# Optimization experiments

Measured on AMD Instinct MI355X. Metric: run time of the kernel, lower is better.

## Reference

```python
import jax, jax.numpy as jnp
import numpy as np

B, N, T, F_IN = 16, 1024, 12, 1
D_MODEL, D_K, D_V, H, K = 512, 32, 32, 3, 3
C = 32  # nb_chev_filter == nb_time_filter


def _ln(x, g, b, eps=1e-5):
    mu = jnp.mean(x, -1, keepdims=True)
    var = jnp.var(x, -1, keepdims=True)
    return (x - mu) * jax.lax.rsqrt(var + eps) * g + b


def _conv(x, w, b):
    y = jax.lax.conv_general_dilated(x, w, (1, 1), 'VALID',
                                     dimension_numbers=('NCHW', 'OIHW', 'NCHW'))
    return y + b[None, :, None, None]


def setup_inputs() -> dict:
    key = jax.random.key(0)
    ks = iter(jax.random.split(key, 40))
    rn = lambda s, sc=0.02: jax.random.normal(next(ks), s, jnp.float32) * sc
    return dict(
        x=rn((B, N, F_IN, T), 1.0),
        res_att=rn((B, F_IN, H, T, T), 0.1),
        pos_embed_T=rn((T, N)),
        gamma_T=jnp.ones((N,)), beta_T=jnp.zeros((N,)),
        WQ_t=rn((N, D_K * H)), WK_t=rn((N, D_K * H)), WV_t=rn((N, D_V * H)),
        fc_t=rn((H * D_V, N)),
        pre_conv_w=rn((D_MODEL, T, 1, F_IN)), pre_conv_b=rn((D_MODEL,)),
        pos_embed_S=rn((N, D_MODEL)),
        gamma_S=jnp.ones((D_MODEL,)), beta_S=jnp.zeros((D_MODEL,)),
        WQ_s=rn((D_MODEL, D_K * K)), WK_s=rn((D_MODEL, D_K * K)),
        cheb_polys=rn((K, N, N), 0.05),
        adj_pa=(jax.random.uniform(next(ks), (N, N)) < 0.01).astype(jnp.float32),
        cheb_mask=rn((K, N, N)),
        Theta=rn((K, F_IN, C), 0.1),
        gtu3_w=rn((2 * C, C, 1, 3)), gtu3_b=rn((2 * C,)),
        gtu5_w=rn((2 * C, C, 1, 5)), gtu5_b=rn((2 * C,)),
        gtu7_w=rn((2 * C, C, 1, 7)), gtu7_b=rn((2 * C,)),
        res_conv_w=rn((C, F_IN, 1, 1)), res_conv_b=rn((C,)),
        fcmy_w=rn((3 * T - 12, T)), fcmy_b=rn((T,)),
        gamma_f=jnp.ones((C,)), beta_f=jnp.zeros((C,)),
    )


def reference(x, res_att, pos_embed_T, gamma_T, beta_T, WQ_t, WK_t, WV_t, fc_t,
              pre_conv_w, pre_conv_b, pos_embed_S, gamma_S, beta_S, WQ_s, WK_s,
              cheb_polys, adj_pa, cheb_mask, Theta,
              gtu3_w, gtu3_b, gtu5_w, gtu5_b, gtu7_w, gtu7_b,
              res_conv_w, res_conv_b, fcmy_w, fcmy_b, gamma_f, beta_f):
    B_, N_, F_, T_ = x.shape
    # ---- temporal embedding (num_of_features == 1 branch): (B,F,T,N) ----
    TEmx = _ln(jnp.transpose(x, (0, 2, 3, 1)) + pos_embed_T[None, None], gamma_T, beta_T)

    # ---- temporal MHA with residual attention bias ----
    def heads(e, W, d):
        y = e @ W  # (B,F,T,H*d)
        return jnp.transpose(y.reshape(B_, F_, T_, H, d), (0, 1, 3, 2, 4))  # (B,F,H,T,d)
    Q, Kt, V = heads(TEmx, WQ_t, D_K), heads(TEmx, WK_t, D_K), heads(TEmx, WV_t, D_V)
    re_At = jnp.einsum('bfhqd,bfhkd->bfhqk', Q, Kt) / np.sqrt(D_K) + res_att
    attn = jax.nn.softmax(re_At, axis=-1)
    ctx = jnp.einsum('bfhqk,bfhkd->bfhqd', attn, V)
    ctx = jnp.transpose(ctx, (0, 1, 3, 2, 4)).reshape(B_, F_, T_, H * D_V)
    one_n, zero_n = jnp.ones((N_,), x.dtype), jnp.zeros((N_,), x.dtype)
    TATout = _ln(ctx @ fc_t + TEmx, one_n, zero_n)  # fresh LayerNorm(d_model) -> gamma=1, beta=0

    # ---- pre_conv: Conv2d(T, d_model, kernel=(1,F)) on (B,T,N,F); take last col ----
    x_TAt = jnp.einsum('btnf,dtf->bnd', jnp.transpose(TATout, (0, 2, 3, 1)),
                       pre_conv_w[:, :, 0, :]) + pre_conv_b  # (B,N,d_model)

    # ---- spatial embedding + spatial attention scores (no softmax) ----
    SEmx = _ln(x_TAt + pos_embed_S[None], gamma_S, beta_S)  # dropout = identity (eval)
    Qs = jnp.transpose((SEmx @ WQ_s).reshape(B_, N_, K, D_K), (0, 2, 1, 3))
    Ks = jnp.transpose((SEmx @ WK_s).reshape(B_, N_, K, D_K), (0, 2, 1, 3))
    STAt = jnp.einsum('bknd,bkmd->bknm', Qs, Ks) / np.sqrt(D_K)  # (B,K,N,N)

    # ---- Chebyshev graph conv weighted by spatial attention ----
    satt = jax.nn.softmax(STAt + (adj_pa[None] * cheb_mask)[None], axis=2)
    Tka = cheb_polys[None] * satt  # (B,K,N,N)
    rhs = jnp.einsum('bkmn,bmft->bknft', Tka, x)  # T_k_with_at^T @ x over all t
    spatial_gcn = jax.nn.relu(jnp.einsum('bknft,kfo->bnot', rhs, Theta))  # (B,N,C,T)

    # ---- gated temporal convs (GTU) ----
    X = jnp.transpose(spatial_gcn, (0, 2, 1, 3))  # (B,C,N,T)
    def gtu(w, b):
        y = _conv(X, w, b)
        return jnp.tanh(y[:, :C]) * jax.nn.sigmoid(y[:, C:])
    time_conv = jnp.concatenate([gtu(gtu3_w, gtu3_b), gtu(gtu5_w, gtu5_b),
                                 gtu(gtu7_w, gtu7_b)], axis=-1)  # (B,C,N,3T-12)
    time_conv = time_conv @ fcmy_w + fcmy_b  # (B,C,N,T)
    tco = jax.nn.relu(time_conv)  # num_of_features == 1 branch

    # ---- residual 1x1 conv + final LayerNorm over channel dim ----
    x_res = _conv(jnp.transpose(x, (0, 2, 1, 3)), res_conv_w, res_conv_b)  # (B,C,N,T)
    out = _ln(jnp.transpose(jax.nn.relu(x_res + tco), (0, 3, 2, 1)), gamma_f, beta_f)
    out = jnp.transpose(out, (0, 2, 3, 1))  # (B,N,C,T)
    return out, re_At
```

## Files before the change

### kernel.cpp

```cpp
#include <hip/hip_runtime.h>
#include <hip/hip_bf16.h>
#include <math.h>

#define B_ 16
#define N_ 1024
#define T_ 12
#define DM_ 512
#define H_ 3
#define K_ 3
#define C_ 32
#define RSQRT_DK 0.17677669529663687f

typedef __attribute__((ext_vector_type(8))) short bf16x8;
typedef __attribute__((ext_vector_type(4))) float f32x4;

__device__ __forceinline__ ushort f2bf(float f) {
  uint u = __float_as_uint(f);
  return (ushort)((u + 0x7FFF + ((u >> 16) & 1)) >> 16);
}
__device__ __forceinline__ float bf2f(ushort h) {
  return __uint_as_float(((uint)h) << 16);
}

__global__ void k1_temporal_ln(const float* __restrict__ x, const float* __restrict__ posT,
                               const float* __restrict__ gT, const float* __restrict__ bT,
                               float* __restrict__ TEmx) {
  int row = blockIdx.x;
  int b = row / T_, t = row - b * T_;
  __shared__ float red[256], red2[256];
  float v[4]; float s = 0.f, s2 = 0.f;
  for (int i = 0; i < 4; ++i) {
    int n = threadIdx.x + (i << 8);
    float val = x[(b * N_ + n) * T_ + t] + posT[t * N_ + n];
    v[i] = val; s += val; s2 += val * val;
  }
  red[threadIdx.x] = s; red2[threadIdx.x] = s2;
  __syncthreads();
  for (int off = 128; off > 0; off >>= 1) {
    if (threadIdx.x < off) { red[threadIdx.x] += red[threadIdx.x + off]; red2[threadIdx.x] += red2[threadIdx.x + off]; }
    __syncthreads();
  }
  float mu = red[0] * (1.f / N_);
  float rs = rsqrtf(red2[0] * (1.f / N_) - mu * mu + 1e-5f);
  for (int i = 0; i < 4; ++i) {
    int n = threadIdx.x + (i << 8);
    TEmx[row * N_ + n] = (v[i] - mu) * rs * gT[n] + bT[n];
  }
}

__global__ __launch_bounds__(256) void k2_qkv(const float* __restrict__ TEmx,
                       const float* __restrict__ WQ, const float* __restrict__ WK,
                       const float* __restrict__ WV, float* __restrict__ part) {
  int kc = blockIdx.x, row = blockIdx.y;
  __shared__ float e[256];
  int tid = threadIdx.x;
  e[tid] = TEmx[row * N_ + kc * 256 + tid];
  __syncthreads();
  for (int col = tid; col < 288; col += 256) {
    int which = col / 96, j = col - which * 96;
    const float* W = (which == 0) ? WQ : ((which == 1) ? WK : WV);
    const float* Wp = W + (size_t)(kc * 256) * 96 + j;
    float acc = 0.f;
    #pragma unroll 8
    for (int n = 0; n < 256; ++n) acc += e[n] * Wp[n * 96];
    part[(row * 4 + kc) * 288 + col] = acc;
  }
}

__global__ __launch_bounds__(256) void k3a_attn(const float* __restrict__ part, const float* __restrict__ res_att,
                         float* __restrict__ reAt_out, float* __restrict__ ctx) {
  int bh = blockIdx.x;
  int b = bh / 3, h = bh - b * 3;
  __shared__ float q_l[3 * T_ * 32];
  __shared__ float s_l[T_ * T_];
  int tid = threadIdx.x;
  for (int i = tid; i < 1152; i += 256) {
    int sec = i / 384, r = i - sec * 384, t = r >> 5, d = r & 31;
    int col = sec * 96 + h * 32 + d;
    const float* pr = &part[(size_t)((b * T_ + t) * 4) * 288 + col];
    q_l[i] = pr[0] + pr[288] + pr[576] + pr[864];
  }
  __syncthreads();
  if (tid < 144) {
    int qi = tid / 12, ki = tid - qi * 12;
    float acc = 0.f;
    #pragma unroll
    for (int d = 0; d < 32; ++d)
      acc += q_l[qi * 32 + d] * q_l[384 + ki * 32 + d];
    float sv = acc * RSQRT_DK + res_att[(size_t)bh * 144 + tid];
    s_l[tid] = sv;
    reAt_out[(size_t)bh * 144 + tid] = sv;
  }
  __syncthreads();
  if (tid < 12) {
    float mx = -1e30f;
    for (int ki = 0; ki < 12; ++ki) mx = fmaxf(mx, s_l[tid * 12 + ki]);
    float sum = 0.f;
    for (int ki = 0; ki < 12; ++ki) { float p = __expf(s_l[tid * 12 + ki] - mx); s_l[tid * 12 + ki] = p; sum += p; }
    float inv = 1.f / sum;
    for (int ki = 0; ki < 12; ++ki) s_l[tid * 12 + ki] *= inv;
  }
  __syncthreads();
  for (int i = tid; i < 384; i += 256) {
    int qi = i >> 5, d = i & 31;
    float acc = 0.f;
    for (int ki = 0; ki < 12; ++ki)
      acc += s_l[qi * 12 + ki] * q_l[768 + ki * 32 + d];
    ctx[(size_t)(b * T_ + qi) * 96 + h * 32 + d] = acc;
  }
}

__global__ __launch_bounds__(1024) void k3b_tat(const float* __restrict__ ctx,
                        const float* __restrict__ fc_t,
                        const float* __restrict__ TEmx, float* __restrict__ TAT) {
  int row = blockIdx.x;
  __shared__ float c_l[96];
  __shared__ float red[16], red2[16];
  int tid = threadIdx.x;
  if (tid < 96) c_l[tid] = ctx[row * 96 + tid];
  __syncthreads();
  float acc = TEmx[row * N_ + tid];
  #pragma unroll 12
  for (int j = 0; j < 96; ++j) acc = fmaf(c_l[j], fc_t[j * N_ + tid], acc);
  float s = acc, s2 = acc * acc;
  #pragma unroll
  for (int off = 32; off > 0; off >>= 1) {
    s  += __shfl_xor(s, off);
    s2 += __shfl_xor(s2, off);
  }
  int w = tid >> 6;
  if ((tid & 63) == 0) { red[w] = s; red2[w] = s2; }
  __syncthreads();
  float ts = 0.f, ts2 = 0.f;
  #pragma unroll
  for (int i = 0; i < 16; ++i) { ts += red[i]; ts2 += red2[i]; }
  float mu = ts * (1.f / N_);
  float rs = rsqrtf(ts2 * (1.f / N_) - mu * mu + 1e-5f);
  TAT[row * N_ + tid] = (acc - mu) * rs;
}

__global__ __launch_bounds__(256) void k_prepack(
    const float* __restrict__ adj, const float* __restrict__ mask,
    const float* __restrict__ cheb, uint* __restrict__ pk,
    const float* __restrict__ WQs, const float* __restrict__ WKs,
    ushort* __restrict__ wpre,
    const float* __restrict__ w3, const float* __restrict__ w5,
    const float* __restrict__ w7, ushort* __restrict__ wg) {
  int bid = blockIdx.x, tid = threadIdx.x;
  if (bid < 3072) {
    int idx = (bid * 256 + tid) * 4;
    int mn = idx & (N_ * N_ - 1);
    float4 a = *(const float4*)&adj[mn];
    float4 m = *(const float4*)&mask[idx];
    float4 c = *(const float4*)&cheb[idx];
    uint4 o;
    o.x = (uint)f2bf(a.x * m.x) | ((uint)f2bf(c.x) << 16);
    o.y = (uint)f2bf(a.y * m.y) | ((uint)f2bf(c.y) << 16);
    o.z = (uint)f2bf(a.z * m.z) | ((uint)f2bf(c.z) << 16);
    o.w = (uint)f2bf(a.w * m.w) | ((uint)f2bf(c.w) << 16);
    *(uint4*)&pk[idx] = o;
  } else if (bid < 3456) {
    int idx = (bid - 3072) * 256 + tid;
    int k = idx / 192, col = idx - k * 192;
    float v = (col < 96) ? WQs[k * 96 + col] : WKs[k * 96 + (col - 96)];
    wpre[col * 512 + k] = f2bf(v);
  } else {
    int idx = (bid - 3456) * 256 + tid;
    if (idx < 6144) {
      int dt = idx / 2048, rem = idx - dt * 2048, co = rem >> 5, ic = rem & 31;
      wg[idx] = f2bf(w3[(co * 32 + ic) * 3 + dt]);
    } else if (idx < 16384) {
      int ds = idx - 6144;
      int dt = ds / 2048, rem = ds - dt * 2048, co = rem >> 5, ic = rem & 31;
      wg[idx] = f2bf(w5[(co * 32 + ic) * 5 + dt]);
    } else if (idx < 30720) {
      int ds = idx - 16384;
      int dt = ds / 2048, rem = ds - dt * 2048, co = rem >> 5, ic = rem & 31;
      wg[idx] = f2bf(w7[(co * 32 + ic) * 7 + dt]);
    }
  }
}

__global__ __launch_bounds__(256) void k5_qks(const float* __restrict__ TAT,
                                              const float* __restrict__ pcw,
                                              const float* __restrict__ pcb,
                                              const float* __restrict__ posS,
                                              const float* __restrict__ gS,
                                              const float* __restrict__ bS,
                                              const ushort* __restrict__ wpre,
                                              __hip_bfloat16* __restrict__ Qs,
                                              __hip_bfloat16* __restrict__ Ks) {
  int b = blockIdx.y, n0 = blockIdx.x * 32;
  __shared__ __align__(16) ushort SE_h[32 * 520];
  int tid = threadIdx.x;
  int w = tid >> 6, lane = tid & 63, quad = (lane >> 4), c16 = lane & 15;

  for (int j = 0; j < 8; ++j) {
    int r = w * 8 + j;
    int n = n0 + r;
    float tc[12];
    #pragma unroll
    for (int t = 0; t < 12; ++t) tc[t] = TAT[(size_t)(b * T_ + t) * N_ + n];
    float vv[8]; float s = 0.f, s2 = 0.f;
    #pragma unroll
    for (int i = 0; i < 8; ++i) {
      int dd = lane + (i << 6);
      const float4* pw = (const float4*)&pcw[dd * 12];
      float4 w0 = pw[0], w1 = pw[1], w2 = pw[2];
      float acc = pcb[dd];
      acc += tc[0] * w0.x + tc[1] * w0.y + tc[2] * w0.z + tc[3] * w0.w;
      acc += tc[4] * w1.x + tc[5] * w1.y + tc[6] * w1.z + tc[7] * w1.w;
      acc += tc[8] * w2.x + tc[9] * w2.y + tc[10] * w2.z + tc[11] * w2.w;
      acc += posS[(size_t)n * DM_ + dd];
      vv[i] = acc; s += acc; s2 += acc * acc;
    }
    #pragma unroll
    for (int off = 1; off < 64; off <<= 1) {
      s  += __shfl_xor(s, off);
      s2 += __shfl_xor(s2, off);
    }
    float mu = s * (1.f / DM_);
    float rs = rsqrtf(s2 * (1.f / DM_) - mu * mu + 1e-5f);
    #pragma unroll
    for (int i = 0; i < 8; ++i) {
      int dd = lane + (i << 6);
      SE_h[r * 520 + dd] = f2bf((vv[i] - mu) * rs * gS[dd] + bS[dd]);
    }
  }
  __syncthreads();

  f32x4 acc[3][2];
  #pragma unroll
  for (int mi = 0; mi < 3; ++mi)
    #pragma unroll
    for (int nt = 0; nt < 2; ++nt) acc[mi][nt] = (f32x4){0.f, 0.f, 0.f, 0.f};

  for (int ks = 0; ks < 16; ++ks) {
    bf16x8 Bf0 = *(const bf16x8*)&SE_h[(0 * 16 + c16) * 520 + ks * 32 + quad * 8];
    bf16x8 Bf1 = *(const bf16x8*)&SE_h[(1 * 16 + c16) * 520 + ks * 32 + quad * 8];
    #pragma unroll
    for (int mi = 0; mi < 3; ++mi) {
      int m = (w * 3 + mi) * 16 + c16;
      bf16x8 Af = *(const bf16x8*)&wpre[m * 512 + ks * 32 + quad * 8];
      acc[mi][0] = __builtin_amdgcn_mfma_f32_16x16x32_bf16(Af, Bf0, acc[mi][0], 0, 0, 0);
      acc[mi][1] = __builtin_amdgcn_mfma_f32_16x16x32_bf16(Af, Bf1, acc[mi][1], 0, 0, 0);
    }
  }
  #pragma unroll
  for (int mi = 0; mi < 3; ++mi) {
    int mb = (w * 3 + mi) * 16;
    #pragma unroll
    for (int nt = 0; nt < 2; ++nt) {
      int node = n0 + nt * 16 + c16;
      #pragma unroll
      for (int r = 0; r < 4; ++r) {
        int m = mb + quad * 4 + r;
        int j = (m < 96) ? m : m - 96;
        int kk = j >> 5, dd = j & 31;
        __hip_bfloat16* o = (m < 96) ? Qs : Ks;
        o[(((b * K_ + kk) * N_) + node) * 32 + dd] = __float2bfloat16(acc[mi][nt][r]);
      }
    }
  }
}

__global__ __launch_bounds__(256) void k6_spatial(
    const __hip_bfloat16* __restrict__ Qs, const __hip_bfloat16* __restrict__ Ks,
    const uint* __restrict__ pk, const float* __restrict__ x,
    float* __restrict__ rhs) {
  const int d  = blockIdx.x;
  const int q_ = d >> 3;
  const int b  = q_ & 15;
  const int g  = ((q_ >> 4) << 3) | (d & 7);
  const int k  = g >> 5;
  const int n0 = (g & 31) << 5;
  const ushort* Qb = (const ushort*)(Qs + (size_t)((b * K_ + k) * N_) * 32);
  const ushort* Kb = (const ushort*)(Ks + (size_t)((b * K_ + k) * N_) * 32);
  const uint* pkk = pk + (size_t)k * (N_ * N_);
  const float* xb = x + b * N_ * T_;

  __shared__ float well[4][32];
  __shared__ float wacc[4][32][12];

  const int tid  = threadIdx.x;
  const int w    = tid >> 6, lane = tid & 63;
  const int quad = lane >> 4, c16 = lane & 15;

  bf16x8 bfr0 = *(const bf16x8*)(Kb + (size_t)(n0 + c16) * 32 + quad * 8);
  bf16x8 bfr1 = *(const bf16x8*)(Kb + (size_t)(n0 + 16 + c16) * 32 + quad * 8);

  float el0 = 0.f, el1 = 0.f;
  float acc0[12], acc1[12];
  #pragma unroll
  for (int t = 0; t < 12; ++t) { acc0[t] = 0.f; acc1[t] = 0.f; }

  for (int s = 0; s < 16; ++s) {
    const int m0 = s * 64 + w * 16;
    bf16x8 af = *(const bf16x8*)(Qb + (size_t)(m0 + c16) * 32 + quad * 8);
    f32x4 z = {0.f, 0.f, 0.f, 0.f};
    f32x4 sc0 = __builtin_amdgcn_mfma_f32_16x16x32_bf16(af, bfr0, z, 0, 0, 0);
    f32x4 sc1 = __builtin_amdgcn_mfma_f32_16x16x32_bf16(af, bfr1, z, 0, 0, 0);

    const int mrow = m0 + quad * 4;
    float p0[4], p1[4];
    #pragma unroll
    for (int r = 0; r < 4; ++r) {
      uint p2 = pkk[(size_t)(mrow + r) * N_ + n0 + c16];
      uint q2 = pkk[(size_t)(mrow + r) * N_ + n0 + 16 + c16];
      float sv0 = sc0[r] * RSQRT_DK + __uint_as_float(p2 << 16);
      float sv1 = sc1[r] * RSQRT_DK + __uint_as_float(q2 << 16);
      p0[r] = __expf(sv0); el0 += p0[r];
      p0[r] *= __uint_as_float(p2 & 0xFFFF0000u);
      p1[r] = __expf(sv1); el1 += p1[r];
      p1[r] *= __uint_as_float(q2 & 0xFFFF0000u);
    }
    #pragma unroll
    for (int r = 0; r < 4; ++r) {
      const float4* xr = (const float4*)(xb + (size_t)(mrow + r) * 12);
      float4 xA = xr[0], xB = xr[1], xC = xr[2];
      float xv[12] = {xA.x, xA.y, xA.z, xA.w, xB.x, xB.y, xB.z, xB.w,
                      xC.x, xC.y, xC.z, xC.w};
      float px0 = p0[r], px1 = p1[r];
      #pragma unroll
      for (int t = 0; t < 12; ++t) {
        acc0[t] = fmaf(px0, xv[t], acc0[t]);
        acc1[t] = fmaf(px1, xv[t], acc1[t]);
      }
    }
  }

  #pragma unroll
  for (int off = 16; off <= 32; off <<= 1) {
    el0 += __shfl_xor(el0, off);
    el1 += __shfl_xor(el1, off);
    #pragma unroll
    for (int t = 0; t < 12; ++t) {
      acc0[t] += __shfl_xor(acc0[t], off);
      acc1[t] += __shfl_xor(acc1[t], off);
    }
  }
  if (quad == 0) {
    well[w][c16] = el0;
    #pragma unroll
    for (int t = 0; t < 12; ++t) wacc[w][c16][t] = acc0[t];
  } else if (quad == 1) {
    well[w][16 + c16] = el1;
    #pragma unroll
    for (int t = 0; t < 12; ++t) wacc[w][16 + c16][t] = acc1[t];
  }
  __syncthreads();
  if (tid < 384) {
    int n = tid / 12, t = tid - n * 12;
    float den = well[0][n] + well[1][n] + well[2][n] + well[3][n];
    float num = wacc[0][n][t] + wacc[1][n][t] + wacc[2][n][t] + wacc[3][n][t];
    rhs[((size_t)(b * K_ + k) * N_ + n0 + n) * 12 + t] = num / den;
  }
}

template<int KS, int JV, int JB, int WOFF>
__device__ __forceinline__ void conv_mfma_g(const ushort* X_th, const ushort* __restrict__ wg,
                                            ushort* tc_h, const float* bias0,
                                            int mp, int ntg, int quad, int c16) {
  f32x4 accA[3], accB[3];
  #pragma unroll
  for (int i = 0; i < 3; ++i) { accA[i] = (f32x4){0.f,0.f,0.f,0.f}; accB[i] = (f32x4){0.f,0.f,0.f,0.f}; }
  #pragma unroll
  for (int dt = 0; dt < KS; ++dt) {
    bf16x8 A0 = *(const bf16x8*)&wg[WOFF + (dt * 64 + mp * 16 + c16) * 32 + quad * 8];
    bf16x8 A1 = *(const bf16x8*)&wg[WOFF + (dt * 64 + (mp + 2) * 16 + c16) * 32 + quad * 8];
    #pragma unroll
    for (int i = 0; i < 3; ++i) {
      int nt = ntg * 3 + i;
      int j = nt >> 1, sh = nt & 1;
      bf16x8 Bf = *(const bf16x8*)&X_th[(sh * 16 + c16) * 584 + (j + dt) * 32 + quad * 8];
      accA[i] = __builtin_amdgcn_mfma_f32_16x16x32_bf16(A0, Bf, accA[i], 0, 0, 0);
      accB[i] = __builtin_amdgcn_mfma_f32_16x16x32_bf16(A1, Bf, accB[i], 0, 0, 0);
    }
  }
  int sxq = ((quad & 1) << 5) ^ ((quad & 2) << 1);
  #pragma unroll
  for (int i = 0; i < 3; ++i) {
    int nt = ntg * 3 + i, j = nt >> 1, sh = nt & 1;
    if (j < JV) {
      int s = sh * 16 + c16;
      int sx = ((s & 15) << 1) ^ sxq;
      #pragma unroll
      for (int r = 0; r < 4; ++r) {
        int cc = mp * 16 + quad * 4 + r;
        float a = accA[i][r] + bias0[cc];
        float g = accB[i][r] + bias0[cc + 32];
        float e2a = __expf(2.f * a);
        float th = 1.f - 2.f / (e2a + 1.f);
        float sg = 1.f / (1.f + __expf(-g));
        tc_h[((s * 32 + cc) * 32 + (JB + j)) ^ sx] = f2bf(th * sg);
      }
    }
  }
}

__global__ __launch_bounds__(1024) void k8_fused(
                       const float* __restrict__ rhs, const float* __restrict__ Theta,
                       const float* __restrict__ x, const float* __restrict__ rw,
                       const float* __restrict__ rb,
                       const ushort* __restrict__ wg,
                       const float* __restrict__ b3, const float* __restrict__ b5,
                       const float* __restrict__ b7,
                       const float* __restrict__ fw, const float* __restrict__ fb,
                       const float* __restrict__ gf, const float* __restrict__ bf,
                       float* __restrict__ out) {
  int bn0 = blockIdx.x * 32;
  int b = bn0 >> 10, n0 = bn0 & 1023;

  __shared__ __align__(16) char uR[50176];
  ushort* X_th = (ushort*)uR;
  float*  v_l  = (float*)uR;
  __shared__ __align__(16) ushort tc_h[1024 * 32];
  __shared__ float rhs_l[32 * 36];
  __shared__ float Th_l[96];
  __shared__ float xr_l[32 * 12];
  __shared__ float fw_l[288];
  __shared__ float fb_l[12];
  __shared__ float bias_l[3][64];
  __shared__ float rw_l[32], rb_l[32], gf_l[32], bf_l[32];
  __shared__ float stm[384], str[384];

  int tid = threadIdx.x;
  int w = tid >> 6, lane = tid & 63, quad = lane >> 4, c16 = lane & 15;
  int mp = w & 1, ntg = w >> 1;
  int c = (tid >> 3) & 31;
  int site = (tid & 7) | ((tid >> 8) << 3);

  for (int idx = tid; idx < 1152; idx += 1024) {
    int s = idx / 36, r = idx - s * 36, k = r / 12, t = r - k * 12;
    rhs_l[idx] = rhs[((size_t)(b * 3 + k) * N_ + n0 + s) * 12 + t];
  }
  if (tid < 384) xr_l[tid] = x[(size_t)(b * N_ + n0) * 12 + tid];
  if (tid < 96) Th_l[tid] = Theta[tid];
  if (tid < 288) fw_l[tid] = fw[tid];
  if (tid < 12) fb_l[tid] = fb[tid];
  if (tid < 64) { bias_l[0][tid] = b3[tid]; bias_l[1][tid] = b5[tid]; bias_l[2][tid] = b7[tid]; }
  if (tid >= 64 && tid < 96)  rw_l[tid - 64] = rw[tid - 64];
  if (tid >= 96 && tid < 128) rb_l[tid - 96] = rb[tid - 96];
  if (tid >= 128 && tid < 160) gf_l[tid - 128] = gf[tid - 128];
  if (tid >= 160 && tid < 192) bf_l[tid - 160] = bf[tid - 160];
  __syncthreads();

  {
    float th0 = Th_l[c], th1 = Th_l[32 + c], th2 = Th_l[64 + c];
    const float* rs_ = &rhs_l[site * 36];
    ushort* xo = &X_th[site * 584 + c];
    #pragma unroll
    for (int t = 0; t < 12; ++t) {
      float a = rs_[t] * th0 + rs_[12 + t] * th1 + rs_[24 + t] * th2;
      xo[t * 32] = f2bf(fmaxf(a, 0.f));
    }
  }
  for (int idx = tid; idx < 32 * 6 * 32; idx += 1024) {
    int s = idx / 192, r2 = idx - s * 192, tt = r2 >> 5, ic = r2 & 31;
    X_th[s * 584 + (12 + tt) * 32 + ic] = 0;
  }
  __syncthreads();

  conv_mfma_g<3, 10, 0,      0>(X_th, wg, tc_h, &bias_l[0][0], mp, ntg, quad, c16);
  conv_mfma_g<5, 8, 10,   6144>(X_th, wg, tc_h, &bias_l[1][0], mp, ntg, quad, c16);
  conv_mfma_g<7, 6, 18,  16384>(X_th, wg, tc_h, &bias_l[2][0], mp, ntg, quad, c16);
  __syncthreads();

  float tcv[24];
  {
    int rb2 = (site * 32 + c) * 32;
    int sxr = ((site & 15) << 1) ^ ((c & 4) << 3) ^ ((c & 8) >> 1);
    #pragma unroll
    for (int j = 0; j < 24; ++j)
      tcv[j] = __uint_as_float(((uint)tc_h[(rb2 + j) ^ sxr]) << 16);
  }
  float o[12];
  #pragma unroll
  for (int t = 0; t < 12; ++t) o[t] = fb_l[t];
  #pragma unroll
  for (int j = 0; j < 24; ++j) {
    const float4* fp = (const float4*)&fw_l[j * 12];
    float4 f0 = fp[0], f1 = fp[1], f2 = fp[2];
    float fr[12] = {f0.x, f0.y, f0.z, f0.w, f1.x, f1.y, f1.z, f1.w, f2.x, f2.y, f2.z, f2.w};
    #pragma unroll
    for (int t = 0; t < 12; ++t) o[t] = fmaf(tcv[j], fr[t], o[t]);
  }

  float v[12];
  {
    float rwc = rw_l[c], rbc = rb_l[c];
    const float* xs = &xr_l[site * 12];
    float* vo = &v_l[site * 391 + c * 12];
    #pragma unroll
    for (int t = 0; t < 12; ++t) {
      float xres = xs[t] * rwc + rbc;
      v[t] = fmaxf(xres + fmaxf(o[t], 0.f), 0.f);
      vo[t] = v[t];
    }
  }
  __syncthreads();
  if (tid < 384) {
    int s = tid / 12, t = tid - s * 12;
    float sm = 0.f, s2 = 0.f;
    #pragma unroll 8
    for (int cc = 0; cc < 32; ++cc) {
      float u = v_l[s * 391 + cc * 12 + t];
      sm += u; s2 += u * u;
    }
    float m = sm * (1.f / 32.f);
    stm[tid] = m;
    str[tid] = rsqrtf(s2 * (1.f / 32.f) - m * m + 1e-5f);
  }
  __syncthreads();
  {
    float gfc = gf_l[c], bfc = bf_l[c];
    const float* sm_ = &stm[site * 12];
    const float* sr_ = &str[site * 12];
    float q[12];
    #pragma unroll
    for (int t = 0; t < 12; ++t) q[t] = (v[t] - sm_[t]) * sr_[t] * gfc + bfc;
    float* op = &out[(size_t)(bn0 + site) * 384 + c * 12];
    ((float4*)op)[0] = make_float4(q[0], q[1], q[2], q[3]);
    ((float4*)op)[1] = make_float4(q[4], q[5], q[6], q[7]);
    ((float4*)op)[2] = make_float4(q[8], q[9], q[10], q[11]);
  }
}

extern "C" void kernel_launch(void* const* d_in, const int* in_sizes, int n_in,
                              void* d_out, int out_size, void* d_ws, size_t ws_size,
                              hipStream_t stream) {
  const float* x       = (const float*)d_in[0];
  const float* res_att = (const float*)d_in[1];
  const float* posT    = (const float*)d_in[2];
  const float* gT      = (const float*)d_in[3];
  const float* bT      = (const float*)d_in[4];
  const float* WQt     = (const float*)d_in[5];
  const float* WKt     = (const float*)d_in[6];
  const float* WVt     = (const float*)d_in[7];
  const float* fct     = (const float*)d_in[8];
  const float* pcw     = (const float*)d_in[9];
  const float* pcb     = (const float*)d_in[10];
  const float* posS    = (const float*)d_in[11];
  const float* gS      = (const float*)d_in[12];
  const float* bS      = (const float*)d_in[13];
  const float* WQs     = (const float*)d_in[14];
  const float* WKs     = (const float*)d_in[15];
  const float* cheb    = (const float*)d_in[16];
  const float* adj     = (const float*)d_in[17];
  const float* mask    = (const float*)d_in[18];
  const float* Theta   = (const float*)d_in[19];
  const float* w3      = (const float*)d_in[20];
  const float* b3      = (const float*)d_in[21];
  const float* w5      = (const float*)d_in[22];
  const float* b5      = (const float*)d_in[23];
  const float* w7      = (const float*)d_in[24];
  const float* b7      = (const float*)d_in[25];
  const float* rw      = (const float*)d_in[26];
  const float* rb      = (const float*)d_in[27];
  const float* fw      = (const float*)d_in[28];
  const float* fb      = (const float*)d_in[29];
  const float* gf      = (const float*)d_in[30];
  const float* bf      = (const float*)d_in[31];

  float* ws = (float*)d_ws;
  float* TEmx = ws;
  float* qkv  = TEmx + 196608;
  float* ctx  = qkv + 55296;
  float* TAT  = ctx + 18432;
  float* SEmx = TAT + 196608;
  float* Qsf  = SEmx + 8388608;
  float* Ksf  = Qsf + 1572864;
  float* rhs  = Ksf + 1572864;
  ushort* wpre = (ushort*)(rhs + 589824);
  ushort* wg   = (ushort*)qkv;
  float* part = SEmx;

  __hip_bfloat16* Qh = (__hip_bfloat16*)Qsf;
  __hip_bfloat16* Kh = (__hip_bfloat16*)Ksf;
  uint* pk = (uint*)(SEmx + 1048576);

  float* out  = (float*)d_out;
  float* reAt = out + 6291456;

  k_prepack<<<3576, 256, 0, stream>>>(adj, mask, cheb, pk, WQs, WKs, wpre,
                                      w3, w5, w7, wg);
  k1_temporal_ln<<<B_ * T_, 256, 0, stream>>>(x, posT, gT, bT, TEmx);
  k2_qkv<<<dim3(4, B_ * T_), 256, 0, stream>>>(TEmx, WQt, WKt, WVt, part);
  k3a_attn<<<B_ * H_, 256, 0, stream>>>(part, res_att, reAt, ctx);
  k3b_tat<<<B_ * T_, 1024, 0, stream>>>(ctx, fct, TEmx, TAT);
  k5_qks<<<dim3(N_ / 32, B_), 256, 0, stream>>>(TAT, pcw, pcb, posS, gS, bS, wpre, Qh, Kh);
  k6_spatial<<<B_ * K_ * (N_ / 32), 256, 0, stream>>>(Qh, Kh, pk, x, rhs);
  k8_fused<<<B_ * N_ / 32, 1024, 0, stream>>>(rhs, Theta, x, rw, rb,
                                              wg, b3, b5, b7, fw, fb, gf, bf, out);
}
```

Measured before the change: 302.4 us.

## Fuse temporal LayerNorm with QKV projection and software-pipeline spatial attention loads

Merges the temporal LayerNorm and QKV projection into one kernel. Each block now computes the full 1024-long dot products from shared memory instead of writing four partial sums that the attention kernel had to add up. This removes a launch and the partial-sum round trip, but the projection now runs on only 192 blocks with 4x longer loops. The spatial attention kernel also gains a two-stage software pipeline that prefetches the next Q fragment and the packed mask/polynomial words before the current MFMA/exp step, plus launch_bounds(256,1), to hide global load latency at the cost of more registers.

Result: slower. 354.3 us (+17.2%).

```diff
diff --git a/kernel.cpp b/kernel.cpp
--- a/kernel.cpp
+++ b/kernel.cpp
@@ -22,52 +22,55 @@
   return __uint_as_float(((uint)h) << 16);
 }
 
-__global__ void k1_temporal_ln(const float* __restrict__ x, const float* __restrict__ posT,
-                               const float* __restrict__ gT, const float* __restrict__ bT,
-                               float* __restrict__ TEmx) {
+__global__ __launch_bounds__(256) void k12_ln_qkv(
+    const float* __restrict__ x, const float* __restrict__ posT,
+    const float* __restrict__ gT, const float* __restrict__ bT,
+    const float* __restrict__ WQ, const float* __restrict__ WK,
+    const float* __restrict__ WV,
+    float* __restrict__ TEmx, float* __restrict__ qkv) {
   int row = blockIdx.x;
   int b = row / T_, t = row - b * T_;
+  __shared__ float e[1024];
   __shared__ float red[256], red2[256];
+  int tid = threadIdx.x;
   float v[4]; float s = 0.f, s2 = 0.f;
   for (int i = 0; i < 4; ++i) {
-    int n = threadIdx.x + (i << 8);
+    int n = tid + (i << 8);
     float val = x[(b * N_ + n) * T_ + t] + posT[t * N_ + n];
     v[i] = val; s += val; s2 += val * val;
   }
-  red[threadIdx.x] = s; red2[threadIdx.x] = s2;
+  red[tid] = s; red2[tid] = s2;
   __syncthreads();
   for (int off = 128; off > 0; off >>= 1) {
-    if (threadIdx.x < off) { red[threadIdx.x] += red[threadIdx.x + off]; red2[threadIdx.x] += red2[threadIdx.x + off]; }
+    if (tid < off) { red[tid] += red[tid + off]; red2[tid] += red2[tid + off]; }
     __syncthreads();
   }
   float mu = red[0] * (1.f / N_);
   float rs = rsqrtf(red2[0] * (1.f / N_) - mu * mu + 1e-5f);
   for (int i = 0; i < 4; ++i) {
-    int n = threadIdx.x + (i << 8);
-    TEmx[row * N_ + n] = (v[i] - mu) * rs * gT[n] + bT[n];
-  }
-}
-
-__global__ __launch_bounds__(256) void k2_qkv(const float* __restrict__ TEmx,
-                       const float* __restrict__ WQ, const float* __restrict__ WK,
-                       const float* __restrict__ WV, float* __restrict__ part) {
-  int kc = blockIdx.x, row = blockIdx.y;
-  __shared__ float e[256];
-  int tid = threadIdx.x;
-  e[tid] = TEmx[row * N_ + kc * 256 + tid];
+    int n = tid + (i << 8);
+    float te = (v[i] - mu) * rs * gT[n] + bT[n];
+    e[n] = te;
+    TEmx[row * N_ + n] = te;
+  }
   __syncthreads();
   for (int col = tid; col < 288; col += 256) {
     int which = col / 96, j = col - which * 96;
     const float* W = (which == 0) ? WQ : ((which == 1) ? WK : WV);
-    const float* Wp = W + (size_t)(kc * 256) * 96 + j;
-    float acc = 0.f;
-    #pragma unroll 8
-    for (int n = 0; n < 256; ++n) acc += e[n] * Wp[n * 96];
-    part[(row * 4 + kc) * 288 + col] = acc;
-  }
-}
-
-__global__ __launch_bounds__(256) void k3a_attn(const float* __restrict__ part, const float* __restrict__ res_att,
+    const float* Wp = W + j;
+    float a0 = 0.f, a1 = 0.f, a2 = 0.f, a3 = 0.f;
+    #pragma unroll 4
+    for (int n = 0; n < 1024; n += 4) {
+      a0 = fmaf(e[n],     Wp[(size_t)n * 96],       a0);
+      a1 = fmaf(e[n + 1], Wp[(size_t)(n + 1) * 96], a1);
+      a2 = fmaf(e[n + 2], Wp[(size_t)(n + 2) * 96], a2);
+      a3 = fmaf(e[n + 3], Wp[(size_t)(n + 3) * 96], a3);
+    }
+    qkv[(size_t)row * 288 + col] = (a0 + a1) + (a2 + a3);
+  }
+}
+
+__global__ __launch_bounds__(256) void k3a_attn(const float* __restrict__ qkv, const float* __restrict__ res_att,
                          float* __restrict__ reAt_out, float* __restrict__ ctx) {
   int bh = blockIdx.x;
   int b = bh / 3, h = bh - b * 3;
@@ -77,8 +80,7 @@
   for (int i = tid; i < 1152; i += 256) {
     int sec = i / 384, r = i - sec * 384, t = r >> 5, d = r & 31;
     int col = sec * 96 + h * 32 + d;
-    const float* pr = &part[(size_t)((b * T_ + t) * 4) * 288 + col];
-    q_l[i] = pr[0] + pr[288] + pr[576] + pr[864];
+    q_l[i] = qkv[(size_t)(b * T_ + t) * 288 + col];
   }
   __syncthreads();
   if (tid < 144) {
@@ -264,7 +266,54 @@
   }
 }
 
-__global__ __launch_bounds__(256) void k6_spatial(
+#define K6_PREF(MM, AF, U0, U1, U2, U3, U4, U5, U6, U7)                        \
+  {                                                                            \
+    int mr_ = (MM) + quad * 4;                                                 \
+    AF = *(const bf16x8*)(Qb + (size_t)((MM) + c16) * 32 + quad * 8);          \
+    U0 = pkk[(size_t)(mr_ + 0) * N_ + n0 + c16];                               \
+    U1 = pkk[(size_t)(mr_ + 1) * N_ + n0 + c16];                               \
+    U2 = pkk[(size_t)(mr_ + 2) * N_ + n0 + c16];                               \
+    U3 = pkk[(size_t)(mr_ + 3) * N_ + n0 + c16];                               \
+    U4 = pkk[(size_t)(mr_ + 0) * N_ + n0 + 16 + c16];                          \
+    U5 = pkk[(size_t)(mr_ + 1) * N_ + n0 + 16 + c16];                          \
+    U6 = pkk[(size_t)(mr_ + 2) * N_ + n0 + 16 + c16];                          \
+    U7 = pkk[(size_t)(mr_ + 3) * N_ + n0 + 16 + c16];                          \
+  }
+
+#define K6_STEP(MM, AF, U0, U1, U2, U3, U4, U5, U6, U7)                        \
+  {                                                                            \
+    f32x4 z_ = {0.f, 0.f, 0.f, 0.f};                                           \
+    f32x4 sc0_ = __builtin_amdgcn_mfma_f32_16x16x32_bf16(AF, bfr0, z_, 0, 0, 0); \
+    f32x4 sc1_ = __builtin_amdgcn_mfma_f32_16x16x32_bf16(AF, bfr1, z_, 0, 0, 0); \
+    uint uu0_[4] = {U0, U1, U2, U3};                                           \
+    uint uu1_[4] = {U4, U5, U6, U7};                                           \
+    float p0_[4], p1_[4];                                                      \
+    _Pragma("unroll")                                                          \
+    for (int r = 0; r < 4; ++r) {                                              \
+      float sv0_ = sc0_[r] * RSQRT_DK + __uint_as_float(uu0_[r] << 16);        \
+      float sv1_ = sc1_[r] * RSQRT_DK + __uint_as_float(uu1_[r] << 16);        \
+      p0_[r] = __expf(sv0_); el0 += p0_[r];                                    \
+      p0_[r] *= __uint_as_float(uu0_[r] & 0xFFFF0000u);                        \
+      p1_[r] = __expf(sv1_); el1 += p1_[r];                                    \
+      p1_[r] *= __uint_as_float(uu1_[r] & 0xFFFF0000u);                        \
+    }                                                                          \
+    int mrow_ = (MM) + quad * 4;                                               \
+    _Pragma("unroll")                                                          \
+    for (int r = 0; r < 4; ++r) {                                              \
+      const float4* xr_ = (const float4*)(xb + (size_t)(mrow_ + r) * 12);      \
+      float4 xA_ = xr_[0], xB_ = xr_[1], xC_ = xr_[2];                         \
+      float xv_[12] = {xA_.x, xA_.y, xA_.z, xA_.w, xB_.x, xB_.y, xB_.z, xB_.w, \
+                       xC_.x, xC_.y, xC_.z, xC_.w};                            \
+      float px0_ = p0_[r], px1_ = p1_[r];                                      \
+      _Pragma("unroll")                                                        \
+      for (int t = 0; t < 12; ++t) {                                           \
+        acc0[t] = fmaf(px0_, xv_[t], acc0[t]);                                 \
+        acc1[t] = fmaf(px1_, xv_[t], acc1[t]);                                 \
+      }                                                                        \
+    }                                                                          \
+  }
+
+__global__ __launch_bounds__(256, 1) void k6_spatial(
     const __hip_bfloat16* __restrict__ Qs, const __hip_bfloat16* __restrict__ Ks,
     const uint* __restrict__ pk, const float* __restrict__ x,
     float* __restrict__ rhs) {
@@ -294,39 +343,17 @@
   #pragma unroll
   for (int t = 0; t < 12; ++t) { acc0[t] = 0.f; acc1[t] = 0.f; }
 
-  for (int s = 0; s < 16; ++s) {
-    const int m0 = s * 64 + w * 16;
-    bf16x8 af = *(const bf16x8*)(Qb + (size_t)(m0 + c16) * 32 + quad * 8);
-    f32x4 z = {0.f, 0.f, 0.f, 0.f};
-    f32x4 sc0 = __builtin_amdgcn_mfma_f32_16x16x32_bf16(af, bfr0, z, 0, 0, 0);
-    f32x4 sc1 = __builtin_amdgcn_mfma_f32_16x16x32_bf16(af, bfr1, z, 0, 0, 0);
-
-    const int mrow = m0 + quad * 4;
-    float p0[4], p1[4];
-    #pragma unroll
-    for (int r = 0; r < 4; ++r) {
-      uint p2 = pkk[(size_t)(mrow + r) * N_ + n0 + c16];
-      uint q2 = pkk[(size_t)(mrow + r) * N_ + n0 + 16 + c16];
-      float sv0 = sc0[r] * RSQRT_DK + __uint_as_float(p2 << 16);
-      float sv1 = sc1[r] * RSQRT_DK + __uint_as_float(q2 << 16);
-      p0[r] = __expf(sv0); el0 += p0[r];
-      p0[r] *= __uint_as_float(p2 & 0xFFFF0000u);
-      p1[r] = __expf(sv1); el1 += p1[r];
-      p1[r] *= __uint_as_float(q2 & 0xFFFF0000u);
-    }
-    #pragma unroll
-    for (int r = 0; r < 4; ++r) {
-      const float4* xr = (const float4*)(xb + (size_t)(mrow + r) * 12);
-      float4 xA = xr[0], xB = xr[1], xC = xr[2];
-      float xv[12] = {xA.x, xA.y, xA.z, xA.w, xB.x, xB.y, xB.z, xB.w,
-                      xC.x, xC.y, xC.z, xC.w};
-      float px0 = p0[r], px1 = p1[r];
-      #pragma unroll
-      for (int t = 0; t < 12; ++t) {
-        acc0[t] = fmaf(px0, xv[t], acc0[t]);
-        acc1[t] = fmaf(px1, xv[t], acc1[t]);
-      }
-    }
+  bf16x8 afA, afB;
+  uint A0, A1, A2, A3, A4, A5, A6, A7;
+  uint B0, B1, B2, B3, B4, B5, B6, B7;
+  K6_PREF(w * 16, afA, A0, A1, A2, A3, A4, A5, A6, A7);
+  for (int s = 0; s < 16; s += 2) {
+    K6_PREF((s + 1) * 64 + w * 16, afB, B0, B1, B2, B3, B4, B5, B6, B7);
+    K6_STEP(s * 64 + w * 16, afA, A0, A1, A2, A3, A4, A5, A6, A7);
+    if (s + 2 < 16) {
+      K6_PREF((s + 2) * 64 + w * 16, afA, A0, A1, A2, A3, A4, A5, A6, A7);
+    }
+    K6_STEP((s + 1) * 64 + w * 16, afB, B0, B1, B2, B3, B4, B5, B6, B7);
   }
 
   #pragma unroll
@@ -564,16 +591,16 @@
 
   float* ws = (float*)d_ws;
   float* TEmx = ws;
-  float* qkv  = TEmx + 196608;
-  float* ctx  = qkv + 55296;
+  float* qkvs = TEmx + 196608;
+  float* ctx  = qkvs + 55296;
   float* TAT  = ctx + 18432;
   float* SEmx = TAT + 196608;
   float* Qsf  = SEmx + 8388608;
   float* Ksf  = Qsf + 1572864;
   float* rhs  = Ksf + 1572864;
   ushort* wpre = (ushort*)(rhs + 589824);
-  ushort* wg   = (ushort*)qkv;
-  float* part = SEmx;
+  ushort* wg   = (ushort*)qkvs;
+  float* qkvp = SEmx;
 
   __hip_bfloat16* Qh = (__hip_bfloat16*)Qsf;
   __hip_bfloat16* Kh = (__hip_bfloat16*)Ksf;
@@ -584,9 +611,8 @@
 
   k_prepack<<<3576, 256, 0, stream>>>(adj, mask, cheb, pk, WQs, WKs, wpre,
                                       w3, w5, w7, wg);
-  k1_temporal_ln<<<B_ * T_, 256, 0, stream>>>(x, posT, gT, bT, TEmx);
-  k2_qkv<<<dim3(4, B_ * T_), 256, 0, stream>>>(TEmx, WQt, WKt, WVt, part);
-  k3a_attn<<<B_ * H_, 256, 0, stream>>>(part, res_att, reAt, ctx);
+  k12_ln_qkv<<<B_ * T_, 256, 0, stream>>>(x, posT, gT, bT, WQt, WKt, WVt, TEmx, qkvp);
+  k3a_attn<<<B_ * H_, 256, 0, stream>>>(qkvp, res_att, reAt, ctx);
   k3b_tat<<<B_ * T_, 1024, 0, stream>>>(ctx, fct, TEmx, TAT);
   k5_qks<<<dim3(N_ / 32, B_), 256, 0, stream>>>(TAT, pcw, pcb, posS, gS, bS, wpre, Qh, Kh);
   k6_spatial<<<B_ * K_ * (N_ / 32), 256, 0, stream>>>(Qh, Kh, pk, x, rhs);
```
